# Optimization experiments

Hardware: AMD Instinct MI355X
Metric: run time of the kernel (lower is better)

Reference implementation:

```python
import jax, jax.numpy as jnp
import numpy as np

D_MODEL = 2048
N_HEADS = 16
D_HEAD = D_MODEL // N_HEADS


def setup_inputs() -> dict:
    key = jax.random.key(0)
    kx, kq, kk, kv, ko = jax.random.split(key, 5)
    s = 1.0 / np.sqrt(D_MODEL)
    return {
        "x": jax.random.normal(kx, (4, 2048, D_MODEL), dtype=jnp.float32),
        "Wq": jax.random.normal(kq, (D_MODEL, D_MODEL), dtype=jnp.float32) * s,
        "Wk": jax.random.normal(kk, (D_MODEL, D_MODEL), dtype=jnp.float32) * s,
        "Wv": jax.random.normal(kv, (D_MODEL, D_MODEL), dtype=jnp.float32) * s,
        "Wo": jax.random.normal(ko, (D_MODEL, D_MODEL), dtype=jnp.float32) * s,
    }


def reference(x, Wq, Wk, Wv, Wo):
    B, S, _ = x.shape
    scale = D_HEAD ** (-0.5)
    # project and split heads: [B, H, S, Dh]
    def split_heads(t):
        return t.reshape(B, S, N_HEADS, D_HEAD).transpose(0, 2, 1, 3)
    q = split_heads(x @ Wq.T)
    k = split_heads(x @ Wk.T)
    v = split_heads(x @ Wv.T)
    sim = jnp.einsum("bhsd,bhtd->bhst", q, k) * scale  # [B,H,S,S]
    causal = jnp.tril(jnp.ones((S, S), dtype=bool))
    sim = jnp.where(causal[None, None], sim, -jnp.inf)
    weights = jax.nn.softmax(sim, axis=-1)
    out = jnp.einsum("bhst,bhtd->bhsd", weights, v)
    out = out.transpose(0, 2, 1, 3).reshape(B, S, D_MODEL)
    return out @ Wo.T
```

## Files before the change

kernel.cpp:

```cpp
#include <hip/hip_runtime.h>

typedef float f32x4 __attribute__((ext_vector_type(4)));
typedef _Float16 f16x8 __attribute__((ext_vector_type(8)));
typedef _Float16 f16x4 __attribute__((ext_vector_type(4)));
typedef unsigned int u32;

#define GLDS16(g, l)                                                        \
  __builtin_amdgcn_global_load_lds(                                         \
      (const __attribute__((address_space(1))) u32*)(g),                    \
      (__attribute__((address_space(3))) u32*)(l), 16, 0, 0)

__global__ void cast_all(const float* __restrict__ x, const float* __restrict__ wq,
                         const float* __restrict__ wk, const float* __restrict__ wv,
                         const float* __restrict__ wo, _Float16* __restrict__ xb,
                         _Float16* __restrict__ wqb, _Float16* __restrict__ wkb,
                         _Float16* __restrict__ wvb, _Float16* __restrict__ wob) {
  const int stride = gridDim.x * blockDim.x;
  const int NX = 4194304;
  const int NW = 1048576;
  for (int i = blockIdx.x * blockDim.x + threadIdx.x; i < NX + 4 * NW; i += stride) {
    const float* src;
    _Float16* dst;
    int off;
    if (i < NX) {
      src = x; dst = xb; off = i;
    } else {
      const int j = i - NX;
      const int s = j >> 20;
      off = j & (NW - 1);
      src = (s == 0) ? wq : (s == 1) ? wk : (s == 2) ? wv : wo;
      dst = (s == 0) ? wqb : (s == 1) ? wkb : (s == 2) ? wvb : wob;
    }
    float4 f = ((const float4*)src)[off];
    f16x4 h = {(_Float16)f.x, (_Float16)f.y, (_Float16)f.z, (_Float16)f.w};
    ((f16x4*)dst)[off] = h;
  }
}

template <int MODE>
__global__ __launch_bounds__(512, 2) void gemm256(
    const _Float16* __restrict__ A, const _Float16* __restrict__ B,
    void* __restrict__ Cout, int M, int N, int K) {
  __shared__ _Float16 SA[2][16384];
  __shared__ _Float16 SB[2][16384];
  const int tid = threadIdx.x;
  const int lane = tid & 63, w = tid >> 6;
  const int l15 = lane & 15, g = lane >> 4;
  const int wm = w >> 2, wn = w & 3;
  const int nbn = N >> 8;
  const int nwg = gridDim.x;
  int bid = blockIdx.x;
  bid = (bid & 7) * (nwg >> 3) + (bid >> 3);
  const int tm = bid / nbn, tn = bid % nbn;

  const _Float16* Ab = A + (size_t)tm * 256 * K;
  const _Float16* Bb = B + (size_t)tn * 256 * K;
  const int rr = tid >> 3;
  const int cx = (lane & 7) ^ (lane >> 3);
  const size_t goff = (size_t)rr * K + cx * 8;
  const int ldst = w * 512;
  const int swz = l15 & 7;

  auto STG_A = [&](int buf, int ha, int rd, int kt) {
    GLDS16(Ab + (size_t)(ha * 128 + rd * 64) * K + kt + goff,
           &SA[buf][ha * 8192 + rd * 4096 + ldst]);
  };
  auto STG_B = [&](int buf, int hb, int rd, int kt) {
    GLDS16(Bb + (size_t)(hb * 128 + rd * 64) * K + kt + goff,
           &SB[buf][hb * 8192 + rd * 4096 + ldst]);
  };

  f32x4 acc[8][4] = {};
  f16x8 a[4][2], b0[2][2], b1[2][2];

  auto LDA = [&](int buf, int mh) {
#pragma unroll
    for (int ml = 0; ml < 4; ++ml)
#pragma unroll
      for (int kk = 0; kk < 2; ++kk)
        a[ml][kk] = *(const f16x8*)(&SA[buf][wm * 8192 + mh * 4096 +
                                             (ml * 16 + l15) * 64 +
                                             ((kk * 4 + g) ^ swz) * 8]);
  };
  auto LDB = [&](int buf, int nh, f16x8 (*bb)[2]) {
#pragma unroll
    for (int nl = 0; nl < 2; ++nl)
#pragma unroll
      for (int kk = 0; kk < 2; ++kk)
        bb[nl][kk] = *(const f16x8*)(&SB[buf][(wn >> 1) * 8192 + (wn & 1) * 4096 +
                                              (nh * 32 + nl * 16 + l15) * 64 +
                                              ((kk * 4 + g) ^ swz) * 8]);
  };
  auto MM = [&](int mh, int nh, f16x8 (*bb)[2]) {
    __builtin_amdgcn_s_setprio(1);
#pragma unroll
    for (int ml = 0; ml < 4; ++ml)
#pragma unroll
      for (int nl = 0; nl < 2; ++nl)
#pragma unroll
        for (int kk = 0; kk < 2; ++kk)
          acc[mh * 4 + ml][nh * 2 + nl] = __builtin_amdgcn_mfma_f32_16x16x32_f16(
              a[ml][kk], bb[nl][kk], acc[mh * 4 + ml][nh * 2 + nl], 0, 0, 0);
    __builtin_amdgcn_s_setprio(0);
  };

  STG_A(0, 0, 0, 0); STG_A(0, 1, 0, 0);
  STG_A(0, 0, 1, 0); STG_A(0, 1, 1, 0);
  STG_B(0, 0, 0, 0); STG_B(0, 0, 1, 0);
  STG_B(0, 1, 0, 0); STG_B(0, 1, 1, 0);
  STG_A(1, 0, 0, 64); STG_A(1, 1, 0, 64);

  const int nit = K >> 7;
  for (int it = 0; it < nit; ++it) {
    const bool lastI = (it == nit - 1);
    const int kq = it * 128 + 64;
    const int kp = it * 128 + 128;
    const int kq2 = it * 128 + 192;
    STG_B(1, 0, 0, kq); STG_B(1, 0, 1, kq);
    asm volatile("s_waitcnt vmcnt(4)\ns_barrier" ::: "memory");
    LDA(0, 0); LDB(0, 0, b0);
    MM(0, 0, b0);
    STG_B(1, 1, 0, kq); STG_B(1, 1, 1, kq);
    asm volatile("s_barrier" ::: "memory");
    LDB(0, 1, b1);
    MM(0, 1, b1);
    STG_A(1, 0, 1, kq); STG_A(1, 1, 1, kq);
    asm volatile("s_barrier" ::: "memory");
    LDA(0, 1);
    MM(1, 0, b0);
    if (!lastI) { STG_A(0, 0, 0, kp); STG_A(0, 1, 0, kp); }
    asm volatile("s_barrier" ::: "memory");
    MM(1, 1, b1);
    if (!lastI) {
      STG_A(0, 0, 1, kp); STG_A(0, 1, 1, kp);
      asm volatile("s_waitcnt vmcnt(6)\ns_barrier" ::: "memory");
    } else {
      asm volatile("s_waitcnt vmcnt(2)\ns_barrier" ::: "memory");
    }
    LDA(1, 0); LDB(1, 0, b0);
    MM(0, 0, b0);
    if (!lastI) { STG_B(0, 0, 0, kp); STG_B(0, 0, 1, kp); }
    asm volatile("s_barrier" ::: "memory");
    LDB(1, 1, b1);
    MM(0, 1, b1);
    if (!lastI) {
      STG_B(0, 1, 0, kp); STG_B(0, 1, 1, kp);
      asm volatile("s_waitcnt vmcnt(8)\ns_barrier" ::: "memory");
    } else {
      asm volatile("s_waitcnt vmcnt(0)\ns_barrier" ::: "memory");
    }
    LDA(1, 1);
    MM(1, 0, b0);
    if (!lastI) { STG_A(1, 0, 0, kq2); STG_A(1, 1, 0, kq2); }
    asm volatile("s_barrier" ::: "memory");
    MM(1, 1, b1);
    asm volatile("s_barrier" ::: "memory");
  }

#pragma unroll
  for (int mi = 0; mi < 8; ++mi) {
#pragma unroll
    for (int ni = 0; ni < 4; ++ni) {
      const int m0 = tm * 256 + wm * 128 + mi * 16 + g * 4;
      const int n = tn * 256 + wn * 64 + ni * 16 + l15;
      if (MODE == 0) {
        _Float16* C = (_Float16*)Cout;
#pragma unroll
        for (int j = 0; j < 4; ++j)
          C[(size_t)(m0 + j) * N + n] = (_Float16)acc[mi][ni][j];
      } else if (MODE == 1) {
        float* C = (float*)Cout;
#pragma unroll
        for (int j = 0; j < 4; ++j)
          C[(size_t)(m0 + j) * N + n] = acc[mi][ni][j];
      } else {
        _Float16* C = (_Float16*)Cout;
        const int bb2 = m0 >> 11, t0 = m0 & 2047;
        const int hh = n >> 7, d = n & 127;
        f16x4 v = {(_Float16)acc[mi][ni][0], (_Float16)acc[mi][ni][1],
                   (_Float16)acc[mi][ni][2], (_Float16)acc[mi][ni][3]};
        *(f16x4*)(C + (size_t)((bb2 * 16 + hh) * 128 + d) * 2048 + t0) = v;
      }
    }
  }
}

__global__ __launch_bounds__(512, 4) void attn_fwd(
    const _Float16* __restrict__ Q, const _Float16* __restrict__ Km,
    const _Float16* __restrict__ VT, _Float16* __restrict__ Aout) {
  __shared__ _Float16 Kl[2][64 * 128];
  __shared__ _Float16 Vl[2][128 * 64];
  __shared__ _Float16 Pl[8][1024];
  const int tid = threadIdx.x;
  const int lane = tid & 63, w = tid >> 6;
  const int l15 = lane & 15, g = lane >> 4;
  const int bid = blockIdx.x;
  const int head = bid & 63;
  const int qt = 15 - (bid >> 6);
  const int b = head >> 4, h = head & 15;
  const int qbase = qt * 128;
  const float SCL2 = 0.12751654f;
  const float MBIAS = 8.6561699f;

  f16x8 qf[4];
  {
    const _Float16* qp =
        Q + (size_t)(b * 2048 + qbase + w * 16 + l15) * 2048 + h * 128 + g * 8;
#pragma unroll
    for (int kk = 0; kk < 4; ++kk) qf[kk] = *(const f16x8*)(qp + kk * 32);
  }
  float l_ = 0.f;
  f32x4 o[8];
  {
    f32x4 z = {0.f, 0.f, 0.f, 0.f};
#pragma unroll
    for (int dt = 0; dt < 8; ++dt) o[dt] = z;
  }

  const int nkv = 2 * (qt + 1);
  auto stageK = [&](int buf, int t) {
    const int kvb = t * 64;
#pragma unroll
    for (int i = 0; i < 2; ++i) {
      const int r = w + i * 8;
      const int c = r * 64 + lane;
      const int tt = c >> 4;
      const int dc = (c & 15) ^ (tt & 15);
      GLDS16(Km + (size_t)(b * 2048 + kvb + tt) * 2048 + h * 128 + dc * 8,
             &Kl[buf][r * 512]);
    }
  };
  auto stageV = [&](int buf, int t) {
    const int kvb = t * 64;
#pragma unroll
    for (int i = 0; i < 2; ++i) {
      const int r = w + i * 8;
      const int c = r * 64 + lane;
      const int d = c >> 3;
      const int tc = (c & 7) ^ (d & 7);
      GLDS16(VT + (size_t)((b * 16 + h) * 128 + d) * 2048 + kvb + tc * 8,
             &Vl[buf][r * 512]);
    }
  };
  stageK(0, 0);
  stageV(0, 0);
  int cur = 0;
  for (int t = 0; t < nkv; ++t) {
    __syncthreads();
    if (t + 1 < nkv) { stageK(cur ^ 1, t + 1); stageV(cur ^ 1, t + 1); }
    const int kvb = t * 64;

    float s[4][4];
#pragma unroll
    for (int kt = 0; kt < 4; ++kt) {
      f32x4 acc = {0.f, 0.f, 0.f, 0.f};
#pragma unroll
      for (int kk = 0; kk < 4; ++kk) {
        const int trow = kt * 16 + l15;
        const int cs = (trow * 16 + kk * 4 + g) ^ (trow & 15);
        f16x8 kf = *(const f16x8*)(&Kl[cur][cs * 8]);
        acc = __builtin_amdgcn_mfma_f32_16x16x32_f16(kf, qf[kk], acc, 0, 0, 0);
      }
#pragma unroll
      for (int j = 0; j < 4; ++j) s[kt][j] = acc[j];
    }
    if (t >= nkv - 2) {
      const int query = qbase + w * 16 + l15;
#pragma unroll
      for (int kt = 0; kt < 4; ++kt)
#pragma unroll
        for (int j = 0; j < 4; ++j)
          if (kvb + kt * 16 + g * 4 + j > query) s[kt][j] = -1e30f;
    }
    _Float16* pl = &Pl[w][0];
#pragma unroll
    for (int kt = 0; kt < 4; ++kt) {
      f16x4 pv;
#pragma unroll
      for (int j = 0; j < 4; ++j) {
        float p = exp2f(s[kt][j] * SCL2 - MBIAS);
        l_ += p;
        pv[j] = (_Float16)p;
      }
      const int c16s = (kt * 2 + (g >> 1)) ^ (l15 & 7);
      *(f16x4*)(pl + l15 * 64 + c16s * 8 + (g & 1) * 4) = pv;
    }
    f16x8 af[2];
    af[0] = *(const f16x8*)(pl + l15 * 64 + ((g ^ (l15 & 7)) * 8));
    af[1] = *(const f16x8*)(pl + l15 * 64 + (((4 + g) ^ (l15 & 7)) * 8));
#pragma unroll
    for (int dt = 0; dt < 8; ++dt) {
#pragma unroll
      for (int kk2 = 0; kk2 < 2; ++kk2) {
        const int d = dt * 16 + l15;
        const int cs = (d * 8 + kk2 * 4 + g) ^ (d & 7);
        f16x8 vf = *(const f16x8*)(&Vl[cur][cs * 8]);
        o[dt] = __builtin_amdgcn_mfma_f32_16x16x32_f16(af[kk2], vf, o[dt], 0, 0, 0);
      }
    }
    __syncthreads();
    cur ^= 1;
  }
  float r = l_;
  r += __shfl_xor(r, 16, 64);
  r += __shfl_xor(r, 32, 64);
  const float rinv = 1.0f / r;
  float inv[4];
#pragma unroll
  for (int j = 0; j < 4; ++j) inv[j] = __shfl(rinv, g * 4 + j, 64);
  const size_t obase =
      (size_t)(b * 2048 + qbase + w * 16 + g * 4) * 2048 + h * 128 + l15;
#pragma unroll
  for (int dt = 0; dt < 8; ++dt)
#pragma unroll
    for (int j = 0; j < 4; ++j)
      Aout[obase + (size_t)j * 2048 + dt * 16] = (_Float16)(o[dt][j] * inv[j]);
}

extern "C" void kernel_launch(void* const* d_in, const int* in_sizes, int n_in,
                              void* d_out, int out_size, void* d_ws, size_t ws_size,
                              hipStream_t stream) {
  const float* x = (const float*)d_in[0];
  const float* Wq = (const float*)d_in[1];
  const float* Wk = (const float*)d_in[2];
  const float* Wv = (const float*)d_in[3];
  const float* Wo = (const float*)d_in[4];
  float* out = (float*)d_out;
  char* ws = (char*)d_ws;

  const size_t SZ_X = 33554432;
  const size_t SZ_W = 8388608;
  _Float16* xb = (_Float16*)(ws);
  _Float16* Wqb = (_Float16*)(ws + SZ_X);
  _Float16* Wkb = (_Float16*)(ws + SZ_X + SZ_W);
  _Float16* Wvb = (_Float16*)(ws + SZ_X + 2 * SZ_W);
  _Float16* Wob = (_Float16*)(ws + SZ_X + 3 * SZ_W);
  _Float16* Qb = (_Float16*)(ws + SZ_X + 4 * SZ_W);
  _Float16* Kb = (_Float16*)(ws + 2 * SZ_X + 4 * SZ_W);
  _Float16* VTb = (_Float16*)(ws + 3 * SZ_X + 4 * SZ_W);
  _Float16* AOb = (_Float16*)(ws + 4 * SZ_X + 4 * SZ_W);

  cast_all<<<4096, 256, 0, stream>>>(x, Wq, Wk, Wv, Wo, xb, Wqb, Wkb, Wvb, Wob);

  const int M = 8192, N = 2048, K = 2048;
  const int grid = (M / 256) * (N / 256);
  gemm256<0><<<grid, 512, 0, stream>>>(xb, Wqb, Qb, M, N, K);
  gemm256<0><<<grid, 512, 0, stream>>>(xb, Wkb, Kb, M, N, K);
  gemm256<2><<<grid, 512, 0, stream>>>(xb, Wvb, VTb, M, N, K);

  attn_fwd<<<1024, 512, 0, stream>>>(Qb, Kb, VTb, AOb);

  gemm256<1><<<grid, 512, 0, stream>>>(AOb, Wob, out, M, N, K);
}
```

Measured before the change: 402.0 us.

## Halve attention KV tile to 32 rows and raise occupancy target

Shrinks the K/V shared-memory tiles and per-wave P buffer from 64 to 32 keys per step and raises launch_bounds min blocks to 8, cutting LDS per block so more blocks can be resident. It also removes the trailing __syncthreads in the KV loop, leaving one barrier per iteration. The double buffer now relies on the top-of-loop barrier alone. The cost is twice as many loop iterations, each with less MFMA work per barrier, and a tighter register budget that could cause spills.

```diff
diff --git a/kernel.cpp b/kernel.cpp
--- a/kernel.cpp
+++ b/kernel.cpp
@@ -185,12 +185,12 @@
   }
 }
 
-__global__ __launch_bounds__(512, 4) void attn_fwd(
+__global__ __launch_bounds__(512, 8) void attn_fwd(
     const _Float16* __restrict__ Q, const _Float16* __restrict__ Km,
     const _Float16* __restrict__ VT, _Float16* __restrict__ Aout) {
-  __shared__ _Float16 Kl[2][64 * 128];
-  __shared__ _Float16 Vl[2][128 * 64];
-  __shared__ _Float16 Pl[8][1024];
+  __shared__ _Float16 Kl[2][32 * 128];
+  __shared__ _Float16 Vl[2][128 * 32];
+  __shared__ _Float16 Pl[8][512];
   const int tid = threadIdx.x;
   const int lane = tid & 63, w = tid >> 6;
   const int l15 = lane & 15, g = lane >> 4;
@@ -217,30 +217,20 @@
     for (int dt = 0; dt < 8; ++dt) o[dt] = z;
   }
 
-  const int nkv = 2 * (qt + 1);
+  const int nkv = 4 * (qt + 1);
   auto stageK = [&](int buf, int t) {
-    const int kvb = t * 64;
-#pragma unroll
-    for (int i = 0; i < 2; ++i) {
-      const int r = w + i * 8;
-      const int c = r * 64 + lane;
-      const int tt = c >> 4;
-      const int dc = (c & 15) ^ (tt & 15);
-      GLDS16(Km + (size_t)(b * 2048 + kvb + tt) * 2048 + h * 128 + dc * 8,
-             &Kl[buf][r * 512]);
-    }
+    const int c = w * 64 + lane;
+    const int tt = c >> 4;
+    const int dc = (c & 15) ^ (tt & 15);
+    GLDS16(Km + (size_t)(b * 2048 + t * 32 + tt) * 2048 + h * 128 + dc * 8,
+           &Kl[buf][w * 512]);
   };
   auto stageV = [&](int buf, int t) {
-    const int kvb = t * 64;
-#pragma unroll
-    for (int i = 0; i < 2; ++i) {
-      const int r = w + i * 8;
-      const int c = r * 64 + lane;
-      const int d = c >> 3;
-      const int tc = (c & 7) ^ (d & 7);
-      GLDS16(VT + (size_t)((b * 16 + h) * 128 + d) * 2048 + kvb + tc * 8,
-             &Vl[buf][r * 512]);
-    }
+    const int c = w * 64 + lane;
+    const int d = c >> 2;
+    const int tc = (c & 3) ^ (d & 3);
+    GLDS16(VT + (size_t)((b * 16 + h) * 128 + d) * 2048 + t * 32 + tc * 8,
+           &Vl[buf][w * 512]);
   };
   stageK(0, 0);
   stageV(0, 0);
@@ -248,33 +238,33 @@
   for (int t = 0; t < nkv; ++t) {
     __syncthreads();
     if (t + 1 < nkv) { stageK(cur ^ 1, t + 1); stageV(cur ^ 1, t + 1); }
-    const int kvb = t * 64;
-
-    float s[4][4];
-#pragma unroll
-    for (int kt = 0; kt < 4; ++kt) {
+
+    float s[2][4];
+#pragma unroll
+    for (int kt = 0; kt < 2; ++kt) {
       f32x4 acc = {0.f, 0.f, 0.f, 0.f};
 #pragma unroll
       for (int kk = 0; kk < 4; ++kk) {
         const int trow = kt * 16 + l15;
-        const int cs = (trow * 16 + kk * 4 + g) ^ (trow & 15);
+        const int cs = trow * 16 + ((kk * 4 + g) ^ (trow & 15));
         f16x8 kf = *(const f16x8*)(&Kl[cur][cs * 8]);
         acc = __builtin_amdgcn_mfma_f32_16x16x32_f16(kf, qf[kk], acc, 0, 0, 0);
       }
 #pragma unroll
       for (int j = 0; j < 4; ++j) s[kt][j] = acc[j];
     }
-    if (t >= nkv - 2) {
+    if (t >= nkv - 4) {
       const int query = qbase + w * 16 + l15;
-#pragma unroll
-      for (int kt = 0; kt < 4; ++kt)
+      const int kvb = t * 32;
+#pragma unroll
+      for (int kt = 0; kt < 2; ++kt)
 #pragma unroll
         for (int j = 0; j < 4; ++j)
           if (kvb + kt * 16 + g * 4 + j > query) s[kt][j] = -1e30f;
     }
     _Float16* pl = &Pl[w][0];
 #pragma unroll
-    for (int kt = 0; kt < 4; ++kt) {
+    for (int kt = 0; kt < 2; ++kt) {
       f16x4 pv;
 #pragma unroll
       for (int j = 0; j < 4; ++j) {
@@ -282,23 +272,17 @@
         l_ += p;
         pv[j] = (_Float16)p;
       }
-      const int c16s = (kt * 2 + (g >> 1)) ^ (l15 & 7);
-      *(f16x4*)(pl + l15 * 64 + c16s * 8 + (g & 1) * 4) = pv;
-    }
-    f16x8 af[2];
-    af[0] = *(const f16x8*)(pl + l15 * 64 + ((g ^ (l15 & 7)) * 8));
-    af[1] = *(const f16x8*)(pl + l15 * 64 + (((4 + g) ^ (l15 & 7)) * 8));
+      const int c16s = (kt * 2 + (g >> 1)) ^ (l15 & 3);
+      *(f16x4*)(pl + l15 * 32 + c16s * 8 + (g & 1) * 4) = pv;
+    }
+    f16x8 af = *(const f16x8*)(pl + l15 * 32 + ((g ^ (l15 & 3)) * 8));
 #pragma unroll
     for (int dt = 0; dt < 8; ++dt) {
-#pragma unroll
-      for (int kk2 = 0; kk2 < 2; ++kk2) {
-        const int d = dt * 16 + l15;
-        const int cs = (d * 8 + kk2 * 4 + g) ^ (d & 7);
-        f16x8 vf = *(const f16x8*)(&Vl[cur][cs * 8]);
-        o[dt] = __builtin_amdgcn_mfma_f32_16x16x32_f16(af[kk2], vf, o[dt], 0, 0, 0);
-      }
-    }
-    __syncthreads();
+      const int d = dt * 16 + l15;
+      const int cs = d * 4 + (g ^ (d & 3));
+      f16x8 vf = *(const f16x8*)(&Vl[cur][cs * 8]);
+      o[dt] = __builtin_amdgcn_mfma_f32_16x16x32_f16(af, vf, o[dt], 0, 0, 0);
+    }
     cur ^= 1;
   }
   float r = l_;
```

Measured after the change: 617.3 us. 53.6% more time.
